# Kernel optimization log

Hardware: AMD Instinct MI355X
Metric: run time of the kernel (lower is better)

Reference implementation:

```python
import jax, jax.numpy as jnp
import numpy as np


def _gen_grid(h, w, stride=1):
    """Normalized spherical sampling grid, shape (3*H', 3*W', 2) with (x, y) order,
    matching gen_grid_coordinates in the torch source (vectorized)."""
    pi = np.pi
    dphi = pi / h
    dth = 2 * pi / w
    t = np.tan(dth)
    p = np.tan(dphi)
    sp = p / np.cos(dth)
    # xys[kr, kc] = (x, y) tangent-plane offsets of the 3x3 kernel taps
    xys = np.array([[[-t, sp], [0.0, p], [t, sp]],
                    [[-t, 0.0], [1.0, 1.0], [t, 0.0]],
                    [[-t, -sp], [0.0, -p], [t, -sp]]], dtype=np.float64)
    X = xys[..., 0]
    Y = xys[..., 1]
    rho = np.sqrt(X ** 2 + Y ** 2)           # [3,3], nonzero everywhere
    v = np.arctan(rho)
    rr = np.arange(0, h, stride)
    cc = np.arange(0, w, stride)
    phi = -((rr + 0.5) / h * pi - pi / 2)    # [H']
    theta = (cc + 0.5) / w * 2 * pi - pi     # [W']
    sphi = np.sin(phi)[:, None, None, None]  # [H',1,1,1]
    cphi = np.cos(phi)[:, None, None, None]
    arg = np.cos(v) * sphi + Y * np.sin(v) * cphi / rho  # [H',1,3,3]
    new_phi = np.arcsin(np.clip(arg, -1.0, 1.0))
    new_theta = theta[None, :, None, None] + np.arctan(
        X * np.sin(v) / (rho * cphi * np.cos(v) - Y * sphi * np.sin(v)))  # [H',W',3,3]
    new_r = np.broadcast_to((-new_phi + pi / 2) * h / pi - 0.5, new_theta.shape).copy()
    new_c = (new_theta + pi) * w / (2 * pi) - 0.5
    new_c = (new_c + w) % w
    # center tap samples the pixel itself
    new_r[:, :, 1, 1] = rr[:, None]
    new_c[:, :, 1, 1] = cc[None, :]
    gx = new_c * 2 / w - 1
    gy = new_r * 2 / h - 1
    grid = np.stack([gx, gy], axis=-1)                     # [H',W',3,3,2]
    Hp, Wp = len(rr), len(cc)
    grid = grid.transpose(0, 2, 1, 3, 4).reshape(Hp * 3, Wp * 3, 2)
    return grid.astype(np.float32)


def _grid_sample_bilinear_zeros(x, grid):
    """torch grid_sample(mode='bilinear', padding_mode='zeros', align_corners=False).
    x: [N,C,H,W]; grid: [Hg,Wg,2] (shared over batch). Returns [N,C,Hg,Wg]."""
    N, C, H, W = x.shape
    ix = ((grid[..., 0] + 1) * W - 1) * 0.5
    iy = ((grid[..., 1] + 1) * H - 1) * 0.5
    x0 = jnp.floor(ix)
    y0 = jnp.floor(iy)
    x1 = x0 + 1
    y1 = y0 + 1
    wx1 = ix - x0
    wx0 = 1.0 - wx1
    wy1 = iy - y0
    wy0 = 1.0 - wy1

    def gather(yy, xx):
        valid = ((xx >= 0) & (xx <= W - 1) & (yy >= 0) & (yy <= H - 1)).astype(x.dtype)
        xi = jnp.clip(xx, 0, W - 1).astype(jnp.int32)
        yi = jnp.clip(yy, 0, H - 1).astype(jnp.int32)
        return x[:, :, yi, xi], valid  # [N,C,Hg,Wg], [Hg,Wg]

    v00, m00 = gather(y0, x0)
    v01, m01 = gather(y0, x1)
    v10, m10 = gather(y1, x0)
    v11, m11 = gather(y1, x1)
    return (v00 * (wy0 * wx0 * m00) + v01 * (wy0 * wx1 * m01)
            + v10 * (wy1 * wx0 * m10) + v11 * (wy1 * wx1 * m11))


def setup_inputs() -> dict:
    key = jax.random.key(0)
    k1, k2, k3 = jax.random.split(key, 3)
    N, Cin, H, W = 4, 64, 128, 256
    Cout = 128
    x = jax.random.normal(k1, (N, Cin, H, W), dtype=jnp.float32)
    fan_in = Cin * 9
    bound = 1.0 / np.sqrt(fan_in)
    weight = jax.random.uniform(k2, (Cout, Cin, 3, 3), dtype=jnp.float32,
                                minval=-bound, maxval=bound)
    bias = jnp.zeros((Cout,), dtype=jnp.float32)
    return {"x": x, "weight": weight, "bias": bias}


def reference(x, weight, bias):
    H, W = int(x.shape[2]), int(x.shape[3])
    grid = jnp.asarray(_gen_grid(H, W, 1))              # [3H, 3W, 2]
    s = _grid_sample_bilinear_zeros(x, grid)            # [N, Cin, 3H, 3W]
    y = jax.lax.conv_general_dilated(
        s, weight, window_strides=(3, 3), padding='VALID',
        dimension_numbers=('NCHW', 'OIHW', 'NCHW'))     # [N, Cout, H, W]
    return y + bias[None, :, None, None]
```

## Files before the change

kernel.cpp:

```cpp
#include <hip/hip_runtime.h>
#include <math.h>

typedef __attribute__((ext_vector_type(8))) short short8;
typedef __attribute__((ext_vector_type(4))) float floatx4;
typedef __attribute__((ext_vector_type(4))) unsigned int uintx4;

#define NB    4
#define CIN   64
#define COUT  128
#define IMH   128
#define IMW   256
#define KTOT  576
#define NPIX  (IMH * IMW)
#define PXT   128
#define NDPB  (PXT * 9)
#define ROWS  4
#define CST   12
#define NCOL  257
#define RST   (NCOL * CST)
#define SLSTR 104
#define KCH   96

__device__ __forceinline__ unsigned short f2bf(float f) {
  union { float f; unsigned u; } v; v.f = f;
  return (unsigned short)((v.u + 0x7FFFu + ((v.u >> 16) & 1u)) >> 16);
}
__device__ __forceinline__ unsigned cvtpk(float lo, float hi) {
  unsigned r;
  asm("v_cvt_pk_bf16_f32 %0, %1, %2" : "=v"(r) : "v"(lo), "v"(hi));
  return r;
}

__global__ __launch_bounds__(256) void prep_w_kernel(const float* __restrict__ w,
                                                     unsigned short* __restrict__ wbf) {
  int idx = blockIdx.x * 256 + threadIdx.x;
  if (idx >= COUT * 8 * KCH) return;
  int co = idx / (8 * KCH);
  int K2 = idx - co * (8 * KCH);
  int cb = K2 / KCH, kk = K2 - cb * KCH;
  unsigned short v = 0;
  if (kk < 72) {
    int t = kk >> 3, chl = kk & 7;
    int ci = cb * 8 + chl;
    v = f2bf(w[co * KTOT + ci * 9 + t]);
  }
  wbf[(K2 >> 3) * (COUT * 8) + co * 8 + (K2 & 7)] = v;
}

__global__ __launch_bounds__(512, 4) void sphconv_kernel(
    const float* __restrict__ x, const unsigned short* __restrict__ wbf,
    const float* __restrict__ bias, float* __restrict__ out) {
  __shared__ __align__(16) float stg[ROWS * RST];
  __shared__ __align__(16) unsigned short Sl[PXT * SLSTR];

  const int tid  = threadIdx.x;
  const int lane = tid & 63;
  const int wv   = tid >> 6;
  const int lin = blockIdx.x + 2 * blockIdx.y;
  const int sw  = (lin & 7) * 32 + (lin >> 3);
  const int ct  = sw >> 7;
  const int r   = sw & 127;
  const int n   = blockIdx.z;
  const int c0  = ct * PXT;
  const int co_base = (wv & 1) * 64;
  const int px_base = (wv >> 1) * 32;
  const int rlo  = min(max(r - 2, 0), IMH - ROWS);
  const int ch   = tid & 7;
  const int colg = tid >> 3;

  const float* xn = x + (size_t)n * CIN * NPIX;

  floatx4 pre[ROWS];
  {
    const float* src = xn + (size_t)ch * NPIX + (size_t)rlo * IMW + colg * 4;
    #pragma unroll
    for (int row = 0; row < ROWS; row++)
      pre[row] = *(const floatx4*)(src + row * IMW);
  }

  int opk[3] = {0, 0, 0}, slw[3] = {0, 0, 0};
  float wq0[3] = {0.f, 0.f, 0.f}, wq1[3] = {0.f, 0.f, 0.f};
  float wq2[3] = {0.f, 0.f, 0.f}, wq3[3] = {0.f, 0.f, 0.f};
  {
    const double pi = 3.14159265358979323846;
    double dphi = pi / IMH;
    double dth  = 2.0 * pi / IMW;
    double t  = tan(dth);
    double p  = tan(dphi);
    double sp = p / cos(dth);
    double phi  = -(((double)r + 0.5) / IMH * pi - pi * 0.5);
    double sphi = sin(phi), cphi = cos(phi);
    #pragma unroll
    for (int dd = 0; dd < 3; dd++) {
      if (dd < 2 || tid < NDPB - 1024) {
        int d  = tid + dd * 512;
        int px = d & (PXT - 1), k = d >> 7;
        int c  = c0 + px;
        int i = k / 3, j = k % 3;
        double theta = ((double)c + 0.5) / IMW * (2.0 * pi) - pi;
        double new_r, new_c;
        if (k == 4) {
          new_r = (double)r; new_c = (double)c;
        } else {
          double X = (j == 0) ? -t : ((j == 2) ? t : 0.0);
          double Y = 0.0;
          if (i == 0)      Y = (j == 1) ?  p :  sp;
          else if (i == 2) Y = (j == 1) ? -p : -sp;
          double rho = sqrt(X * X + Y * Y);
          double v   = atan(rho);
          double sv = sin(v), cv = cos(v);
          double arg = cv * sphi + Y * sv * cphi / rho;
          arg = fmin(1.0, fmax(-1.0, arg));
          double new_phi = asin(arg);
          double denom = rho * cphi * cv - Y * sphi * sv;
          double new_theta = theta + atan(X * sv / denom);
          new_r = (-new_phi + pi * 0.5) * IMH / pi - 0.5;
          new_c = (new_theta + pi) * IMW / (2.0 * pi) - 0.5;
          new_c = fmod(new_c + (double)IMW, (double)IMW);
        }
        float gx = (float)(new_c * 2.0 / IMW - 1.0);
        float gy = (float)(new_r * 2.0 / IMH - 1.0);
        float ix = ((gx + 1.0f) * (float)IMW - 1.0f) * 0.5f;
        float iy = ((gy + 1.0f) * (float)IMH - 1.0f) * 0.5f;
        float fx = floorf(ix), fy = floorf(iy);
        int x0 = (int)fx, y0 = (int)fy;
        float wx1 = ix - fx, wy1 = iy - fy;
        float wx0 = 1.0f - wx1, wy0 = 1.0f - wy1;
        int x1 = x0 + 1, y1 = y0 + 1;
        bool vy0 = (y0 >= 0) & (y0 <= IMH - 1);
        bool vy1 = (y1 >= 0) & (y1 <= IMH - 1);
        int y0c = min(max(y0, 0), IMH - 1), y1c = min(max(y1, 0), IMH - 1);
        int x0c = max(x0, 0);
        float w_lo = (x0 >= 0) ? wx0 : wx1;
        float w_hi = (x0 >= 0) ? ((x1 <= IMW - 1) ? wx1 : 0.0f) : 0.0f;
        float wy0m = vy0 ? wy0 : 0.0f, wy1m = vy1 ? wy1 : 0.0f;
        int rt = min(max(y0c - rlo, 0), ROWS - 1);
        int rb = min(max(y1c - rlo, 0), ROWS - 1);
        opk[dd] = (rt * RST + x0c * CST) | ((rb * RST + x0c * CST) << 16);
        wq0[dd] = wy0m * w_lo; wq1[dd] = wy0m * w_hi;
        wq2[dd] = wy1m * w_lo; wq3[dd] = wy1m * w_hi;
        slw[dd] = px * (SLSTR / 2) + k * 4;
      }
    }
  }

  {
    float* dch = &stg[(colg * 4) * CST + ch];
    #pragma unroll
    for (int row = 0; row < ROWS; row++) {
      floatx4 v = pre[row];
      float* dr = dch + row * RST;
      dr[0] = v.x; dr[CST] = v.y; dr[2 * CST] = v.z; dr[3 * CST] = v.w;
    }
  }
  if (tid < 32) stg[(tid >> 3) * RST + 256 * CST + (tid & 7)] = 0.0f;
  #pragma unroll
  for (int z = 0; z < 3; z++) {
    int q = tid + z * 512;
    int px = q / 12;
    ((unsigned int*)Sl)[px * 52 + 36 + (q - px * 12)] = 0u;
  }

  floatx4 acc[4][2];
  #pragma unroll
  for (int mt = 0; mt < 4; mt++)
    #pragma unroll
    for (int nt = 0; nt < 2; nt++)
      acc[mt][nt] = (floatx4){0.f, 0.f, 0.f, 0.f};

  __syncthreads();

  #pragma unroll 1
  for (int cb = 0; cb < 8; cb++) {
    #pragma unroll
    for (int dd = 0; dd < 3; dd++) {
      if (dd < 2 || tid < NDPB - 1024) {
        unsigned op = (unsigned)opk[dd];
        const float* pt = &stg[op & 0xFFFFu];
        const float* pb = &stg[op >> 16];
        floatx4 t0  = *(const floatx4*)(pt);
        floatx4 t0h = *(const floatx4*)(pt + 4);
        floatx4 t1  = *(const floatx4*)(pt + CST);
        floatx4 t1h = *(const floatx4*)(pt + CST + 4);
        floatx4 b0  = *(const floatx4*)(pb);
        floatx4 b0h = *(const floatx4*)(pb + 4);
        floatx4 b1  = *(const floatx4*)(pb + CST);
        floatx4 b1h = *(const floatx4*)(pb + CST + 4);
        float w0 = wq0[dd], w1 = wq1[dd], w2 = wq2[dd], w3 = wq3[dd];
        floatx4 slo = t0 * w0 + t1 * w1 + b0 * w2 + b1 * w3;
        floatx4 shi = t0h * w0 + t1h * w1 + b0h * w2 + b1h * w3;
        uintx4 U;
        U.x = cvtpk(slo.x, slo.y); U.y = cvtpk(slo.z, slo.w);
        U.z = cvtpk(shi.x, shi.y); U.w = cvtpk(shi.z, shi.w);
        *(uintx4*)((unsigned int*)Sl + slw[dd]) = U;
      }
    }
    __syncthreads();
    if (cb < 7) {
      const float* src = xn + (size_t)((cb + 1) * 8 + ch) * NPIX + (size_t)rlo * IMW + colg * 4;
      float* dch = &stg[(colg * 4) * CST + ch];
      #pragma unroll
      for (int row = 0; row < ROWS; row++) {
        floatx4 v = *(const floatx4*)(src + row * IMW);
        float* dr = dch + row * RST;
        dr[0] = v.x; dr[CST] = v.y; dr[2 * CST] = v.z; dr[3 * CST] = v.w;
      }
    }
    #pragma unroll
    for (int ks = 0; ks < 3; ks++) {
      const unsigned short* arow =
          wbf + (size_t)((cb * 12 + ks * 4 + (lane >> 4)) * COUT + co_base + (lane & 15)) * 8;
      #pragma unroll
      for (int nt = 0; nt < 2; nt++) {
        short8 b = *(const short8*)&Sl[(px_base + nt * 16 + (lane & 15)) * SLSTR
                                       + ks * 32 + (lane >> 4) * 8];
        #pragma unroll
        for (int mt = 0; mt < 4; mt++) {
          short8 a = *(const short8*)(arow + mt * 16 * 8);
          acc[mt][nt] = __builtin_amdgcn_mfma_f32_16x16x32_bf16(a, b, acc[mt][nt], 0, 0, 0);
        }
      }
    }
    __syncthreads();
  }

  #pragma unroll
  for (int mt = 0; mt < 4; mt++)
    #pragma unroll
    for (int nt = 0; nt < 2; nt++)
      #pragma unroll
      for (int rg = 0; rg < 4; rg++) {
        const int co = co_base + mt * 16 + (lane >> 4) * 4 + rg;
        const int cc = c0 + px_base + nt * 16 + (lane & 15);
        out[(((size_t)n * COUT + co) * IMH + r) * IMW + cc] = acc[mt][nt][rg] + bias[co];
      }
}

extern "C" void kernel_launch(void* const* d_in, const int* in_sizes, int n_in,
                              void* d_out, int out_size, void* d_ws, size_t ws_size,
                              hipStream_t stream) {
  const float* x    = (const float*)d_in[0];
  const float* w    = (const float*)d_in[1];
  const float* bias = (const float*)d_in[2];
  float* out = (float*)d_out;
  unsigned short* wbf = (unsigned short*)d_ws;
  (void)in_sizes; (void)n_in; (void)out_size; (void)ws_size;

  hipLaunchKernelGGL(prep_w_kernel, dim3((COUT * 8 * KCH + 255) / 256), dim3(256), 0, stream, w, wbf);
  hipLaunchKernelGGL(sphconv_kernel, dim3(IMW / PXT, IMH, NB), dim3(512), 0, stream,
                     x, wbf, bias, out);
}
```

Baseline: 169.9 us.

## Switch staging and MFMA to fp16, precompute per-tap row math once per block

Changes the x staging buffer from fp32 to packed fp16 pairs with a bank-swizzle, and does the bilinear interpolation in packed half arithmetic. MFMA moves from bf16 to f16. The per-row trig for each of the 9 taps is now computed once by nine threads and shared through LDS, which removes most of the double-precision work each thread did per sample. Global loads for the next channel block are issued at the top of the loop to overlap with interpolation. The change also raises the occupancy hint and adds s_setprio around the MFMA section. Doing the interpolation in fp16 with round-toward-zero weights adds precision risk.

New measurement: 324.8 us. +91.2%, slower.

```diff
diff --git a/kernel.cpp b/kernel.cpp
--- a/kernel.cpp
+++ b/kernel.cpp
@@ -2,6 +2,9 @@
 #include <math.h>
 
 typedef __attribute__((ext_vector_type(8))) short short8;
+typedef __attribute__((ext_vector_type(8))) _Float16 half8;
+typedef __attribute__((ext_vector_type(4))) _Float16 half4;
+typedef __attribute__((ext_vector_type(2))) _Float16 half2;
 typedef __attribute__((ext_vector_type(4))) float floatx4;
 typedef __attribute__((ext_vector_type(4))) unsigned int uintx4;
 
@@ -15,20 +18,20 @@
 #define PXT   128
 #define NDPB  (PXT * 9)
 #define ROWS  4
-#define CST   12
+#define CSTW  6
 #define NCOL  257
-#define RST   (NCOL * CST)
+#define RSTW  (NCOL * CSTW)
 #define SLSTR 104
 #define KCH   96
 
-__device__ __forceinline__ unsigned short f2bf(float f) {
-  union { float f; unsigned u; } v; v.f = f;
-  return (unsigned short)((v.u + 0x7FFFu + ((v.u >> 16) & 1u)) >> 16);
-}
-__device__ __forceinline__ unsigned cvtpk(float lo, float hi) {
+__device__ __forceinline__ unsigned pkrtz2(float a, float b) {
   unsigned r;
-  asm("v_cvt_pk_bf16_f32 %0, %1, %2" : "=v"(r) : "v"(lo), "v"(hi));
+  asm("v_cvt_pkrtz_f16_f32 %0, %1, %2" : "=v"(r) : "v"(a), "v"(b));
   return r;
+}
+__device__ __forceinline__ half4 dup4(unsigned u) {
+  half2 h; __builtin_memcpy(&h, &u, 4);
+  return __builtin_shufflevector(h, h, 0, 1, 0, 1);
 }
 
 __global__ __launch_bounds__(256) void prep_w_kernel(const float* __restrict__ w,
@@ -42,16 +45,20 @@
   if (kk < 72) {
     int t = kk >> 3, chl = kk & 7;
     int ci = cb * 8 + chl;
-    v = f2bf(w[co * KTOT + ci * 9 + t]);
+    _Float16 h = (_Float16)w[co * KTOT + ci * 9 + t];
+    __builtin_memcpy(&v, &h, 2);
   }
   wbf[(K2 >> 3) * (COUT * 8) + co * 8 + (K2 & 7)] = v;
 }
 
-__global__ __launch_bounds__(512, 4) void sphconv_kernel(
+__global__ __launch_bounds__(512, 6) void sphconv_kernel(
     const float* __restrict__ x, const unsigned short* __restrict__ wbf,
     const float* __restrict__ bias, float* __restrict__ out) {
-  __shared__ __align__(16) float stg[ROWS * RST];
+  __shared__ __align__(16) unsigned int stg[ROWS * RSTW];
   __shared__ __align__(16) unsigned short Sl[PXT * SLSTR];
+  __shared__ double tapA[9];
+  __shared__ float  tapWy[9][2];
+  __shared__ int    tapRo[9][2];
 
   const int tid  = threadIdx.x;
   const int lane = tid & 63;
@@ -65,95 +72,124 @@
   const int co_base = (wv & 1) * 64;
   const int px_base = (wv >> 1) * 32;
   const int rlo  = min(max(r - 2, 0), IMH - ROWS);
-  const int ch   = tid & 7;
-  const int colg = tid >> 3;
+  const int sp  = tid & 3;
+  const int scg = (tid >> 2) & 63;
+  const int srr = tid >> 8;
 
   const float* xn = x + (size_t)n * CIN * NPIX;
 
-  floatx4 pre[ROWS];
+  floatx4 nx[4];
+  #pragma unroll
+  for (int c = 0; c < 2; c++)
+    #pragma unroll
+    for (int rw = 0; rw < 2; rw++)
+      nx[c * 2 + rw] = *(const floatx4*)(xn + (size_t)(sp * 2 + c) * NPIX
+                                         + (size_t)(rlo + srr * 2 + rw) * IMW + scg * 4);
+
   {
-    const float* src = xn + (size_t)ch * NPIX + (size_t)rlo * IMW + colg * 4;
-    #pragma unroll
-    for (int row = 0; row < ROWS; row++)
-      pre[row] = *(const floatx4*)(src + row * IMW);
-  }
+    int myk = -1;
+    if (lane == 0) myk = wv;
+    if (wv == 0 && lane == 32) myk = 8;
+    if (myk >= 0) {
+      const double pi = 3.14159265358979323846;
+      double dphi = pi / IMH;
+      double dth  = 2.0 * pi / IMW;
+      double t  = tan(dth);
+      double p  = tan(dphi);
+      double sp_ = p / cos(dth);
+      double phi  = -(((double)r + 0.5) / IMH * pi - pi * 0.5);
+      double sphi = sin(phi), cphi = cos(phi);
+      int i = myk / 3, j = myk % 3;
+      double atv, new_r;
+      if (myk == 4) {
+        atv = 0.0; new_r = (double)r;
+      } else {
+        double X = (j == 0) ? -t : ((j == 2) ? t : 0.0);
+        double Y = 0.0;
+        if (i == 0)      Y = (j == 1) ?  p :  sp_;
+        else if (i == 2) Y = (j == 1) ? -p : -sp_;
+        double rho = sqrt(X * X + Y * Y);
+        double v   = atan(rho);
+        double sv = sin(v), cv = cos(v);
+        double arg = cv * sphi + Y * sv * cphi / rho;
+        arg = fmin(1.0, fmax(-1.0, arg));
+        double new_phi = asin(arg);
+        double denom = rho * cphi * cv - Y * sphi * sv;
+        atv = atan(X * sv / denom);
+        new_r = (-new_phi + pi * 0.5) * IMH / pi - 0.5;
+      }
+      float gy = (float)(new_r * 2.0 / IMH - 1.0);
+      float iy = ((gy + 1.0f) * (float)IMH - 1.0f) * 0.5f;
+      float fy = floorf(iy); int y0 = (int)fy;
+      float wy1 = iy - fy, wy0 = 1.0f - wy1;
+      int y1 = y0 + 1;
+      bool vy0 = (y0 >= 0) & (y0 <= IMH - 1);
+      bool vy1 = (y1 >= 0) & (y1 <= IMH - 1);
+      int y0c = min(max(y0, 0), IMH - 1), y1c = min(max(y1, 0), IMH - 1);
+      int rt = min(max(y0c - rlo, 0), ROWS - 1);
+      int rb = min(max(y1c - rlo, 0), ROWS - 1);
+      tapA[myk] = atv;
+      tapWy[myk][0] = vy0 ? wy0 : 0.0f;
+      tapWy[myk][1] = vy1 ? wy1 : 0.0f;
+      tapRo[myk][0] = rt * RSTW;
+      tapRo[myk][1] = rb * RSTW;
+    }
+  }
+  __syncthreads();
 
   int opk[3] = {0, 0, 0}, slw[3] = {0, 0, 0};
-  float wq0[3] = {0.f, 0.f, 0.f}, wq1[3] = {0.f, 0.f, 0.f};
-  float wq2[3] = {0.f, 0.f, 0.f}, wq3[3] = {0.f, 0.f, 0.f};
+  unsigned uq0[3] = {0,0,0}, uq1[3] = {0,0,0}, uq2[3] = {0,0,0}, uq3[3] = {0,0,0};
   {
     const double pi = 3.14159265358979323846;
-    double dphi = pi / IMH;
-    double dth  = 2.0 * pi / IMW;
-    double t  = tan(dth);
-    double p  = tan(dphi);
-    double sp = p / cos(dth);
-    double phi  = -(((double)r + 0.5) / IMH * pi - pi * 0.5);
-    double sphi = sin(phi), cphi = cos(phi);
     #pragma unroll
     for (int dd = 0; dd < 3; dd++) {
       if (dd < 2 || tid < NDPB - 1024) {
         int d  = tid + dd * 512;
         int px = d & (PXT - 1), k = d >> 7;
         int c  = c0 + px;
-        int i = k / 3, j = k % 3;
-        double theta = ((double)c + 0.5) / IMW * (2.0 * pi) - pi;
-        double new_r, new_c;
+        double nc;
         if (k == 4) {
-          new_r = (double)r; new_c = (double)c;
+          nc = (double)c;
         } else {
-          double X = (j == 0) ? -t : ((j == 2) ? t : 0.0);
-          double Y = 0.0;
-          if (i == 0)      Y = (j == 1) ?  p :  sp;
-          else if (i == 2) Y = (j == 1) ? -p : -sp;
-          double rho = sqrt(X * X + Y * Y);
-          double v   = atan(rho);
-          double sv = sin(v), cv = cos(v);
-          double arg = cv * sphi + Y * sv * cphi / rho;
-          arg = fmin(1.0, fmax(-1.0, arg));
-          double new_phi = asin(arg);
-          double denom = rho * cphi * cv - Y * sphi * sv;
-          double new_theta = theta + atan(X * sv / denom);
-          new_r = (-new_phi + pi * 0.5) * IMH / pi - 0.5;
-          new_c = (new_theta + pi) * IMW / (2.0 * pi) - 0.5;
-          new_c = fmod(new_c + (double)IMW, (double)IMW);
+          double theta = ((double)c + 0.5) / IMW * (2.0 * pi) - pi;
+          double new_theta = theta + tapA[k];
+          nc = (new_theta + pi) * IMW / (2.0 * pi) - 0.5;
+          nc = fmod(nc + (double)IMW, (double)IMW);
         }
-        float gx = (float)(new_c * 2.0 / IMW - 1.0);
-        float gy = (float)(new_r * 2.0 / IMH - 1.0);
+        float gx = (float)(nc * 2.0 / IMW - 1.0);
         float ix = ((gx + 1.0f) * (float)IMW - 1.0f) * 0.5f;
-        float iy = ((gy + 1.0f) * (float)IMH - 1.0f) * 0.5f;
-        float fx = floorf(ix), fy = floorf(iy);
-        int x0 = (int)fx, y0 = (int)fy;
-        float wx1 = ix - fx, wy1 = iy - fy;
-        float wx0 = 1.0f - wx1, wy0 = 1.0f - wy1;
-        int x1 = x0 + 1, y1 = y0 + 1;
-        bool vy0 = (y0 >= 0) & (y0 <= IMH - 1);
-        bool vy1 = (y1 >= 0) & (y1 <= IMH - 1);
-        int y0c = min(max(y0, 0), IMH - 1), y1c = min(max(y1, 0), IMH - 1);
+        float fx = floorf(ix); int x0 = (int)fx;
+        float wx1 = ix - fx, wx0 = 1.0f - wx1;
+        int x1 = x0 + 1;
         int x0c = max(x0, 0);
         float w_lo = (x0 >= 0) ? wx0 : wx1;
         float w_hi = (x0 >= 0) ? ((x1 <= IMW - 1) ? wx1 : 0.0f) : 0.0f;
-        float wy0m = vy0 ? wy0 : 0.0f, wy1m = vy1 ? wy1 : 0.0f;
-        int rt = min(max(y0c - rlo, 0), ROWS - 1);
-        int rb = min(max(y1c - rlo, 0), ROWS - 1);
-        opk[dd] = (rt * RST + x0c * CST) | ((rb * RST + x0c * CST) << 16);
-        wq0[dd] = wy0m * w_lo; wq1[dd] = wy0m * w_hi;
-        wq2[dd] = wy1m * w_lo; wq3[dd] = wy1m * w_hi;
-        slw[dd] = px * (SLSTR / 2) + k * 4;
-      }
-    }
-  }
-
-  {
-    float* dch = &stg[(colg * 4) * CST + ch];
-    #pragma unroll
-    for (int row = 0; row < ROWS; row++) {
-      floatx4 v = pre[row];
-      float* dr = dch + row * RST;
-      dr[0] = v.x; dr[CST] = v.y; dr[2 * CST] = v.z; dr[3 * CST] = v.w;
-    }
-  }
-  if (tid < 32) stg[(tid >> 3) * RST + 256 * CST + (tid & 7)] = 0.0f;
+        float wy0m = tapWy[k][0], wy1m = tapWy[k][1];
+        float w0 = wy0m * w_lo, w1 = wy0m * w_hi;
+        float w2 = wy1m * w_lo, w3 = wy1m * w_hi;
+        int sh0 = ((x0c >> 4) & 1) * 2;
+        int sh1 = (((x0c + 1) >> 4) & 1) * 2;
+        int dc  = CSTW + sh1 - sh0;
+        int offt = tapRo[k][0] + x0c * CSTW + sh0;
+        int offb = tapRo[k][1] + x0c * CSTW + sh0;
+        opk[dd] = offt | (offb << 16);
+        slw[dd] = (px * (SLSTR / 2) + k * 4) | (dc << 16);
+        uq0[dd] = pkrtz2(w0, w0); uq1[dd] = pkrtz2(w1, w1);
+        uq2[dd] = pkrtz2(w2, w2); uq3[dd] = pkrtz2(w3, w3);
+      }
+    }
+  }
+
+  #pragma unroll
+  for (int rw = 0; rw < 2; rw++)
+    #pragma unroll
+    for (int i = 0; i < 4; i++) {
+      int col = scg * 4 + i;
+      int sh = ((col >> 4) & 1) * 2;
+      stg[(srr * 2 + rw) * RSTW + col * CSTW + sh + sp] =
+          pkrtz2(nx[rw][i], nx[2 + rw][i]);
+    }
+  if (tid < 16) stg[(tid >> 2) * RSTW + 256 * CSTW + (tid & 3)] = 0u;
   #pragma unroll
   for (int z = 0; z < 3; z++) {
     int q = tid + z * 512;
@@ -172,55 +208,68 @@
 
   #pragma unroll 1
   for (int cb = 0; cb < 8; cb++) {
+    if (cb < 7) {
+      #pragma unroll
+      for (int c = 0; c < 2; c++)
+        #pragma unroll
+        for (int rw = 0; rw < 2; rw++)
+          nx[c * 2 + rw] = *(const floatx4*)(xn + (size_t)((cb + 1) * 8 + sp * 2 + c) * NPIX
+                                             + (size_t)(rlo + srr * 2 + rw) * IMW + scg * 4);
+    }
     #pragma unroll
     for (int dd = 0; dd < 3; dd++) {
       if (dd < 2 || tid < NDPB - 1024) {
         unsigned op = (unsigned)opk[dd];
-        const float* pt = &stg[op & 0xFFFFu];
-        const float* pb = &stg[op >> 16];
-        floatx4 t0  = *(const floatx4*)(pt);
-        floatx4 t0h = *(const floatx4*)(pt + 4);
-        floatx4 t1  = *(const floatx4*)(pt + CST);
-        floatx4 t1h = *(const floatx4*)(pt + CST + 4);
-        floatx4 b0  = *(const floatx4*)(pb);
-        floatx4 b0h = *(const floatx4*)(pb + 4);
-        floatx4 b1  = *(const floatx4*)(pb + CST);
-        floatx4 b1h = *(const floatx4*)(pb + CST + 4);
-        float w0 = wq0[dd], w1 = wq1[dd], w2 = wq2[dd], w3 = wq3[dd];
-        floatx4 slo = t0 * w0 + t1 * w1 + b0 * w2 + b1 * w3;
-        floatx4 shi = t0h * w0 + t1h * w1 + b0h * w2 + b1h * w3;
-        uintx4 U;
-        U.x = cvtpk(slo.x, slo.y); U.y = cvtpk(slo.z, slo.w);
-        U.z = cvtpk(shi.x, shi.y); U.w = cvtpk(shi.z, shi.w);
-        *(uintx4*)((unsigned int*)Sl + slw[dd]) = U;
+        const unsigned* pt = stg + (op & 0xFFFFu);
+        const unsigned* pb = stg + (op >> 16);
+        int dc = slw[dd] >> 16;
+        half4 t0  = *(const half4*)(pt);
+        half4 t0h = *(const half4*)(pt + 2);
+        half4 t1  = *(const half4*)(pt + dc);
+        half4 t1h = *(const half4*)(pt + dc + 2);
+        half4 b0  = *(const half4*)(pb);
+        half4 b0h = *(const half4*)(pb + 2);
+        half4 b1  = *(const half4*)(pb + dc);
+        half4 b1h = *(const half4*)(pb + dc + 2);
+        half4 W0 = dup4(uq0[dd]), W1 = dup4(uq1[dd]);
+        half4 W2 = dup4(uq2[dd]), W3 = dup4(uq3[dd]);
+        half4 slo = t0 * W0 + t1 * W1 + b0 * W2 + b1 * W3;
+        half4 shi = t0h * W0 + t1h * W1 + b0h * W2 + b1h * W3;
+        union { half4 h; unsigned u[2]; } ua, ub;
+        ua.h = slo; ub.h = shi;
+        uintx4 U = {ua.u[0], ua.u[1], ub.u[0], ub.u[1]};
+        *(uintx4*)((unsigned int*)Sl + (slw[dd] & 0xFFFF)) = U;
       }
     }
     __syncthreads();
     if (cb < 7) {
-      const float* src = xn + (size_t)((cb + 1) * 8 + ch) * NPIX + (size_t)rlo * IMW + colg * 4;
-      float* dch = &stg[(colg * 4) * CST + ch];
       #pragma unroll
-      for (int row = 0; row < ROWS; row++) {
-        floatx4 v = *(const floatx4*)(src + row * IMW);
-        float* dr = dch + row * RST;
-        dr[0] = v.x; dr[CST] = v.y; dr[2 * CST] = v.z; dr[3 * CST] = v.w;
-      }
-    }
+      for (int rw = 0; rw < 2; rw++)
+        #pragma unroll
+        for (int i = 0; i < 4; i++) {
+          int col = scg * 4 + i;
+          int sh = ((col >> 4) & 1) * 2;
+          stg[(srr * 2 + rw) * RSTW + col * CSTW + sh + sp] =
+              pkrtz2(nx[rw][i], nx[2 + rw][i]);
+        }
+    }
+    __builtin_amdgcn_s_setprio(1);
     #pragma unroll
     for (int ks = 0; ks < 3; ks++) {
       const unsigned short* arow =
           wbf + (size_t)((cb * 12 + ks * 4 + (lane >> 4)) * COUT + co_base + (lane & 15)) * 8;
       #pragma unroll
       for (int nt = 0; nt < 2; nt++) {
-        short8 b = *(const short8*)&Sl[(px_base + nt * 16 + (lane & 15)) * SLSTR
-                                       + ks * 32 + (lane >> 4) * 8];
+        half8 b = *(const half8*)&Sl[(px_base + nt * 16 + (lane & 15)) * SLSTR
+                                     + ks * 32 + (lane >> 4) * 8];
         #pragma unroll
         for (int mt = 0; mt < 4; mt++) {
-          short8 a = *(const short8*)(arow + mt * 16 * 8);
-          acc[mt][nt] = __builtin_amdgcn_mfma_f32_16x16x32_bf16(a, b, acc[mt][nt], 0, 0, 0);
+          half8 a = *(const half8*)(arow + mt * 16 * 8);
+          acc[mt][nt] = __builtin_amdgcn_mfma_f32_16x16x32_f16(a, b, acc[mt][nt], 0, 0, 0);
         }
       }
     }
+    __builtin_amdgcn_s_setprio(0);
     __syncthreads();
   }
 
```
